# Kernel tuning notes

Hardware: AMD Instinct MI355X
Metric: run time of the kernel (lower is better)

The kernel has to match this reference:

```python
import jax, jax.numpy as jnp
import numpy as np

B = 8192
D_LS, D_A, D_LM, D_AT, D_DS, D_DM = 1024, 512, 512, 512, 1024, 512
LENGTH = D_LS + D_A + D_LM  # 2048
OUT = 512


def setup_inputs() -> dict:
    key = jax.random.key(0)
    ks = jax.random.split(key, 9)
    return {
        "result_ls": jax.random.normal(ks[0], (B, 1, D_LS), jnp.float32),
        "result_A": jax.random.normal(ks[1], (B, 1, D_A), jnp.float32),
        "result_lm": jax.random.normal(ks[2], (B, 1, D_LM), jnp.float32),
        "result_AT": jax.random.normal(ks[3], (B, 1, D_AT), jnp.float32),
        "result_ds": jax.random.normal(ks[4], (B, 1, D_DS), jnp.float32),
        "result_dm": jax.random.normal(ks[5], (B, 1, D_DM), jnp.float32),
        "W": jax.random.normal(ks[6], (OUT, LENGTH), jnp.float32) * (1.0 / np.sqrt(LENGTH)),
        "b": jax.random.normal(ks[7], (OUT,), jnp.float32) * 0.01,
        "h_n": jax.random.normal(ks[8], (OUT, 1), jnp.float32) * (1.0 / np.sqrt(OUT)),
    }


def _pad_to(x, length):
    # zero-pad last dim of [B,1,d] to [B,1,length]
    return jnp.pad(x, ((0, 0), (0, 0), (0, length - x.shape[2])))


def reference(result_ls, result_A, result_lm, result_AT, result_ds, result_dm, W, b, h_n):
    # pad each node-type feature to common length and stack along node axis -> [B,6,L]
    nodes = jnp.concatenate(
        [_pad_to(t, LENGTH) for t in (result_ls, result_A, result_lm, result_AT, result_ds, result_dm)],
        axis=1,
    )
    temp = jnp.tanh(jnp.einsum("bnl,ol->bno", nodes, W) + b)  # [B,6,OUT]
    score = jnp.einsum("bno,oi->bni", temp, h_n)               # [B,6,1]
    score = score.reshape(-1, 1, 6)
    beta = jax.nn.softmax(score, axis=2)                        # [B,1,6]
    z_i = jnp.matmul(beta, nodes)                               # [B,1,L]
    return z_i
```

## Files before the change

kernel.cpp:

```cpp
#include <hip/hip_runtime.h>
#include <hip/hip_bf16.h>
#include <stdint.h>

typedef __attribute__((ext_vector_type(8))) short bf16x8;
typedef __attribute__((ext_vector_type(4))) float f32x4;

#define NB 8192

__device__ __forceinline__ unsigned short f2bf(float f) {
    unsigned int u = __float_as_uint(f);
    u += 0x7fffu + ((u >> 16) & 1u);
    return (unsigned short)(u >> 16);
}

__device__ __forceinline__ uint4 pack8(float4 a, float4 b) {
    uint4 r;
    r.x = (unsigned)f2bf(a.x) | ((unsigned)f2bf(a.y) << 16);
    r.y = (unsigned)f2bf(a.z) | ((unsigned)f2bf(a.w) << 16);
    r.z = (unsigned)f2bf(b.x) | ((unsigned)f2bf(b.y) << 16);
    r.w = (unsigned)f2bf(b.z) | ((unsigned)f2bf(b.w) << 16);
    return r;
}

__global__ __launch_bounds__(256)
void prep_w_kernel(const float* __restrict__ W, uint4* __restrict__ Wt) {
    int t = blockIdx.x * 256 + threadIdx.x;
    int lane = t & 63;
    int frag = t >> 6;
    int kb = frag >> 5, cb = frag & 31;
    int o = cb * 16 + (lane & 15);
    int k = kb * 32 + ((lane >> 4) << 3);
    const float* src = W + (size_t)o * 2048 + k;
    float4 a = *(const float4*)src;
    float4 b = *(const float4*)(src + 4);
    Wt[t] = pack8(a, b);
}

__global__ __launch_bounds__(512, 4)
void score_kernel(const float* __restrict__ x0, const float* __restrict__ x1,
                  const float* __restrict__ x2, const float* __restrict__ x3,
                  const float* __restrict__ x4, const float* __restrict__ x5,
                  const float* __restrict__ bias, const float* __restrict__ hvec,
                  const uint4* __restrict__ Wt, float* __restrict__ scores) {
    __shared__ uint4 lA[2][256];
    __shared__ float red[8][64];

    int bid = blockIdx.x;
    int node = bid % 6;
    int tile = bid / 6;
    const float* xp; int dn;
    switch (node) {
        case 0: xp = x0; dn = 1024; break;
        case 1: xp = x1; dn = 512;  break;
        case 2: xp = x2; dn = 512;  break;
        case 3: xp = x3; dn = 512;  break;
        case 4: xp = x4; dn = 1024; break;
        default: xp = x5; dn = 512; break;
    }
    int m0 = tile * 64;
    int t = threadIdx.x;
    int lane = t & 63;
    int w = t >> 6;

    int sl = (t >> 1) & 63;
    int h = t & 1;
    int srow = (t >> 7) * 16 + (sl & 15);
    int scol = ((sl >> 4) << 3) + (h << 2);
    const float* sp = xp + (size_t)(m0 + srow) * dn + scol;

    int nsteps = dn >> 5;

    {
        float4 a = *(const float4*)sp;
        uint2 p;
        p.x = (unsigned)f2bf(a.x) | ((unsigned)f2bf(a.y) << 16);
        p.y = (unsigned)f2bf(a.z) | ((unsigned)f2bf(a.w) << 16);
        ((uint2*)&lA[0][0])[t] = p;
    }
    __syncthreads();

    f32x4 acc[4][4];
#pragma unroll
    for (int mf = 0; mf < 4; ++mf)
#pragma unroll
        for (int nf = 0; nf < 4; ++nf)
            acc[mf][nf] = (f32x4){0.f, 0.f, 0.f, 0.f};

    int cur = 0;
    for (int s = 0; s < nsteps; ++s) {
        float4 na;
        bool hn = (s + 1) < nsteps;
        if (hn) na = *(const float4*)(sp + (s + 1) * 32);

        const uint4* wp = Wt + ((size_t)((s << 5) + (w << 2)) << 6) + lane;
        bf16x8 bfr[4];
#pragma unroll
        for (int nf = 0; nf < 4; ++nf)
            bfr[nf] = __builtin_bit_cast(bf16x8, wp[nf << 6]);
        bf16x8 afr[4];
#pragma unroll
        for (int mf = 0; mf < 4; ++mf)
            afr[mf] = __builtin_bit_cast(bf16x8, lA[cur][(mf << 6) + lane]);
#pragma unroll
        for (int mf = 0; mf < 4; ++mf)
#pragma unroll
            for (int nf = 0; nf < 4; ++nf)
                acc[mf][nf] = __builtin_amdgcn_mfma_f32_16x16x32_bf16(
                    afr[mf], bfr[nf], acc[mf][nf], 0, 0, 0);
        if (hn) {
            uint2 p;
            p.x = (unsigned)f2bf(na.x) | ((unsigned)f2bf(na.y) << 16);
            p.y = (unsigned)f2bf(na.z) | ((unsigned)f2bf(na.w) << 16);
            ((uint2*)&lA[cur ^ 1][0])[t] = p;
        }
        __syncthreads();
        cur ^= 1;
    }

    float bv[4], hv[4];
#pragma unroll
    for (int nf = 0; nf < 4; ++nf) {
        int o = (w << 6) + (nf << 4) + (lane & 15);
        bv[nf] = bias[o];
        hv[nf] = hvec[o];
    }
#pragma unroll
    for (int mf = 0; mf < 4; ++mf) {
        float sc[4] = {0.f, 0.f, 0.f, 0.f};
#pragma unroll
        for (int nf = 0; nf < 4; ++nf) {
#pragma unroll
            for (int r = 0; r < 4; ++r) {
                float xv = acc[mf][nf][r] + bv[nf];
                float th = 1.f - 2.f * __builtin_amdgcn_rcpf(1.f + __expf(2.f * xv));
                sc[r] = fmaf(hv[nf], th, sc[r]);
            }
        }
#pragma unroll
        for (int r = 0; r < 4; ++r) {
            float v = sc[r];
            v += __shfl_xor(v, 1);
            v += __shfl_xor(v, 2);
            v += __shfl_xor(v, 4);
            v += __shfl_xor(v, 8);
            if ((lane & 15) == 0)
                red[w][(mf << 4) + ((lane >> 4) << 2) + r] = v;
        }
    }
    __syncthreads();
    if (t < 64) {
        float ssum = 0.f;
#pragma unroll
        for (int w2 = 0; w2 < 8; ++w2) ssum += red[w2][t];
        scores[node * NB + m0 + t] = ssum;
    }
}

__global__ __launch_bounds__(256)
void z_kernel(const float* __restrict__ x0, const float* __restrict__ x1,
              const float* __restrict__ x2, const float* __restrict__ x3,
              const float* __restrict__ x4, const float* __restrict__ x5,
              const float* __restrict__ scores, float* __restrict__ out) {
    int wv = threadIdx.x >> 6;
    int lane = threadIdx.x & 63;
    int b = (blockIdx.x << 2) + wv;

    float s0 = scores[b];
    float s1 = scores[NB + b];
    float s2 = scores[2 * NB + b];
    float s3 = scores[3 * NB + b];
    float s4 = scores[4 * NB + b];
    float s5 = scores[5 * NB + b];
    float m = fmaxf(fmaxf(fmaxf(s0, s1), fmaxf(s2, s3)), fmaxf(s4, s5));
    float e0 = __expf(s0 - m), e1 = __expf(s1 - m), e2 = __expf(s2 - m);
    float e3 = __expf(s3 - m), e4 = __expf(s4 - m), e5 = __expf(s5 - m);
    float inv = __builtin_amdgcn_rcpf(e0 + e1 + e2 + e3 + e4 + e5);
    float b0 = e0 * inv, b1 = e1 * inv, b2 = e2 * inv;
    float b3 = e3 * inv, b4 = e4 * inv, b5 = e5 * inv;

    const float* pls = x0 + (size_t)b * 1024;
    const float* pA  = x1 + (size_t)b * 512;
    const float* plm = x2 + (size_t)b * 512;
    const float* pAT = x3 + (size_t)b * 512;
    const float* pds = x4 + (size_t)b * 1024;
    const float* pdm = x5 + (size_t)b * 512;
    float* po = out + (size_t)b * 2048;

#pragma unroll
    for (int j = 0; j < 2; ++j) {
        int c = (j << 8) + (lane << 2);
        float4 vls = *(const float4*)(pls + c);
        float4 vA  = *(const float4*)(pA + c);
        float4 vlm = *(const float4*)(plm + c);
        float4 vAT = *(const float4*)(pAT + c);
        float4 vds = *(const float4*)(pds + c);
        float4 vdm = *(const float4*)(pdm + c);
        float4 r;
        r.x = b0*vls.x + b1*vA.x + b2*vlm.x + b3*vAT.x + b4*vds.x + b5*vdm.x;
        r.y = b0*vls.y + b1*vA.y + b2*vlm.y + b3*vAT.y + b4*vds.y + b5*vdm.y;
        r.z = b0*vls.z + b1*vA.z + b2*vlm.z + b3*vAT.z + b4*vds.z + b5*vdm.z;
        r.w = b0*vls.w + b1*vA.w + b2*vlm.w + b3*vAT.w + b4*vds.w + b5*vdm.w;
        *(float4*)(po + c) = r;
    }
#pragma unroll
    for (int j = 0; j < 2; ++j) {
        int c = 512 + (j << 8) + (lane << 2);
        float4 vls = *(const float4*)(pls + c);
        float4 vds = *(const float4*)(pds + c);
        float4 r;
        r.x = b0*vls.x + b4*vds.x;
        r.y = b0*vls.y + b4*vds.y;
        r.z = b0*vls.z + b4*vds.z;
        r.w = b0*vls.w + b4*vds.w;
        *(float4*)(po + c) = r;
    }
    float4 zz = make_float4(0.f, 0.f, 0.f, 0.f);
#pragma unroll
    for (int j = 0; j < 4; ++j) {
        int c = 1024 + (j << 8) + (lane << 2);
        *(float4*)(po + c) = zz;
    }
}

extern "C" void kernel_launch(void* const* d_in, const int* in_sizes, int n_in,
                              void* d_out, int out_size, void* d_ws, size_t ws_size,
                              hipStream_t stream) {
    const float* x0   = (const float*)d_in[0];
    const float* x1   = (const float*)d_in[1];
    const float* x2   = (const float*)d_in[2];
    const float* x3   = (const float*)d_in[3];
    const float* x4   = (const float*)d_in[4];
    const float* x5   = (const float*)d_in[5];
    const float* W    = (const float*)d_in[6];
    const float* bias = (const float*)d_in[7];
    const float* hvec = (const float*)d_in[8];

    uint4* Wt = (uint4*)d_ws;
    float* scores = (float*)((char*)d_ws + (1u << 20));

    prep_w_kernel<<<256, 256, 0, stream>>>(W, Wt);
    score_kernel<<<768, 512, 0, stream>>>(x0, x1, x2, x3, x4, x5, bias, hvec, Wt, scores);
    z_kernel<<<2048, 256, 0, stream>>>(x0, x1, x2, x3, x4, x5, scores, (float*)d_out);
}
```

Before: 108.9 us.

## Stream fp32 activations into swizzled LDS via direct global-to-LDS loads

The score kernel now uses global_load_lds to copy fp32 activation tiles straight into a double-buffered, XOR-swizzled LDS buffer covering 64 K per step. Each wave converts to bf16 after reading from LDS, using the packed hardware conversion. This removes the register round trip and the per-thread convert-and-store before the barrier, and halves the number of barriers. In exchange, LDS use grows to 32KB per block and the conversion work is repeated by every wave that reads a fragment.

```diff
diff --git a/kernel.cpp b/kernel.cpp
--- a/kernel.cpp
+++ b/kernel.cpp
@@ -7,19 +7,26 @@
 
 #define NB 8192
 
-__device__ __forceinline__ unsigned short f2bf(float f) {
-    unsigned int u = __float_as_uint(f);
-    u += 0x7fffu + ((u >> 16) & 1u);
-    return (unsigned short)(u >> 16);
+__device__ __forceinline__ unsigned pkbf(float x, float y) {
+    __hip_bfloat162 h = __float22bfloat162_rn(make_float2(x, y));
+    unsigned r;
+    __builtin_memcpy(&r, &h, 4);
+    return r;
 }
 
 __device__ __forceinline__ uint4 pack8(float4 a, float4 b) {
     uint4 r;
-    r.x = (unsigned)f2bf(a.x) | ((unsigned)f2bf(a.y) << 16);
-    r.y = (unsigned)f2bf(a.z) | ((unsigned)f2bf(a.w) << 16);
-    r.z = (unsigned)f2bf(b.x) | ((unsigned)f2bf(b.y) << 16);
-    r.w = (unsigned)f2bf(b.z) | ((unsigned)f2bf(b.w) << 16);
+    r.x = pkbf(a.x, a.y);
+    r.y = pkbf(a.z, a.w);
+    r.z = pkbf(b.x, b.y);
+    r.w = pkbf(b.z, b.w);
     return r;
+}
+
+__device__ __forceinline__ void gload_lds16(const float* g, void* l) {
+    __builtin_amdgcn_global_load_lds(
+        (const __attribute__((address_space(1))) void*)g,
+        (__attribute__((address_space(3))) void*)l, 16, 0, 0);
 }
 
 __global__ __launch_bounds__(256)
@@ -42,7 +49,7 @@
                   const float* __restrict__ x4, const float* __restrict__ x5,
                   const float* __restrict__ bias, const float* __restrict__ hvec,
                   const uint4* __restrict__ Wt, float* __restrict__ scores) {
-    __shared__ uint4 lA[2][256];
+    __shared__ uint4 lA[2][1024];
     __shared__ float red[8][64];
 
     int bid = blockIdx.x;
@@ -62,21 +69,20 @@
     int lane = t & 63;
     int w = t >> 6;
 
-    int sl = (t >> 1) & 63;
-    int h = t & 1;
-    int srow = (t >> 7) * 16 + (sl & 15);
-    int scol = ((sl >> 4) << 3) + (h << 2);
-    const float* sp = xp + (size_t)(m0 + srow) * dn + scol;
-
-    int nsteps = dn >> 5;
-
-    {
-        float4 a = *(const float4*)sp;
-        uint2 p;
-        p.x = (unsigned)f2bf(a.x) | ((unsigned)f2bf(a.y) << 16);
-        p.y = (unsigned)f2bf(a.z) | ((unsigned)f2bf(a.w) << 16);
-        ((uint2*)&lA[0][0])[t] = p;
-    }
+    int nst = dn >> 6;
+
+    int ra = ((w << 1) + 0) * 4 + (lane >> 4);
+    int rb = ((w << 1) + 1) * 4 + (lane >> 4);
+    int sa = (lane & 15) ^ (ra & 7);
+    int sb = (lane & 15) ^ (rb & 7);
+    const float* ga = xp + (size_t)(m0 + ra) * dn + (sa << 2);
+    const float* gb = xp + (size_t)(m0 + rb) * dn + (sb << 2);
+    char* lbaseA = (char*)&lA[0][0] + (((w << 1) + 0) << 10);
+    char* lbaseB = (char*)&lA[0][0] + (((w << 1) + 1) << 10);
+
+    gload_lds16(ga, lbaseA);
+    gload_lds16(gb, lbaseB);
+    ga += 64; gb += 64;
     __syncthreads();
 
     f32x4 acc[4][4];
@@ -86,35 +92,43 @@
         for (int nf = 0; nf < 4; ++nf)
             acc[mf][nf] = (f32x4){0.f, 0.f, 0.f, 0.f};
 
-    int cur = 0;
-    for (int s = 0; s < nsteps; ++s) {
-        float4 na;
-        bool hn = (s + 1) < nsteps;
-        if (hn) na = *(const float4*)(sp + (s + 1) * 32);
-
-        const uint4* wp = Wt + ((size_t)((s << 5) + (w << 2)) << 6) + lane;
-        bf16x8 bfr[4];
-#pragma unroll
-        for (int nf = 0; nf < 4; ++nf)
-            bfr[nf] = __builtin_bit_cast(bf16x8, wp[nf << 6]);
-        bf16x8 afr[4];
-#pragma unroll
-        for (int mf = 0; mf < 4; ++mf)
-            afr[mf] = __builtin_bit_cast(bf16x8, lA[cur][(mf << 6) + lane]);
-#pragma unroll
-        for (int mf = 0; mf < 4; ++mf)
-#pragma unroll
-            for (int nf = 0; nf < 4; ++nf)
-                acc[mf][nf] = __builtin_amdgcn_mfma_f32_16x16x32_bf16(
-                    afr[mf], bfr[nf], acc[mf][nf], 0, 0, 0);
-        if (hn) {
-            uint2 p;
-            p.x = (unsigned)f2bf(na.x) | ((unsigned)f2bf(na.y) << 16);
-            p.y = (unsigned)f2bf(na.z) | ((unsigned)f2bf(na.w) << 16);
-            ((uint2*)&lA[cur ^ 1][0])[t] = p;
+    const char* ldsroot = (const char*)&lA[0][0];
+
+    for (int s = 0; s < nst; ++s) {
+        int cur = s & 1;
+        if (s + 1 < nst) {
+            gload_lds16(ga, lbaseA + ((cur ^ 1) << 14));
+            gload_lds16(gb, lbaseB + ((cur ^ 1) << 14));
+            ga += 64; gb += 64;
+        }
+#pragma unroll
+        for (int ks = 0; ks < 2; ++ks) {
+            int kblock = (s << 1) + ks;
+            const uint4* wp = Wt + (((kblock << 5) + (w << 2)) << 6) + lane;
+            bf16x8 bfr[4];
+#pragma unroll
+            for (int nf = 0; nf < 4; ++nf) {
+                uint4 u = wp[nf << 6];
+                __builtin_memcpy(&bfr[nf], &u, 16);
+            }
+#pragma unroll
+            for (int mf = 0; mf < 4; ++mf) {
+                int r = (mf << 4) + (lane & 15);
+                int slot = (ks << 3) + ((lane >> 4) << 1);
+                int sw = r & 7;
+                const char* p = ldsroot + (cur << 14) + (r << 8);
+                float4 lo = *(const float4*)(p + (((slot) ^ sw) << 4));
+                float4 hi = *(const float4*)(p + (((slot + 1) ^ sw) << 4));
+                uint4 pk = pack8(lo, hi);
+                bf16x8 afr;
+                __builtin_memcpy(&afr, &pk, 16);
+#pragma unroll
+                for (int nf = 0; nf < 4; ++nf)
+                    acc[mf][nf] = __builtin_amdgcn_mfma_f32_16x16x32_bf16(
+                        afr, bfr[nf], acc[mf][nf], 0, 0, 0);
+            }
         }
         __syncthreads();
-        cur ^= 1;
     }
 
     float bv[4], hv[4];
```

Measured after the change: 114.0 us. +4.7%, slower.
